# Kernel tuning notes

Hardware: AMD Instinct MI355X
Metric: run time of the kernel (lower is better)

## Reference

```python
import jax, jax.numpy as jnp
import numpy as np

N_HEAD, D_K, D_V, D_MODEL = 12, 64, 64, 768
SMOOTH = 1e-06
LN_EPS = 1e-06


def _layer_norm(x, g, b, eps=LN_EPS):
    m = x.mean(-1, keepdims=True)
    v = x.var(-1, keepdims=True)
    return (x - m) / jnp.sqrt(v + eps) * g + b


def setup_inputs() -> dict:
    key = jax.random.key(0)
    ks = jax.random.split(key, 12)
    b, L, R = 4, 1024, 97
    w = lambda k, i, o: jax.random.normal(k, (i, o), jnp.float32) * 0.02
    return {
        'doc_input': jax.random.normal(ks[0], (b, L, D_MODEL), jnp.float32),
        'rel_input': jax.random.normal(ks[1], (b, R, D_MODEL), jnp.float32),
        'mask': jax.random.randint(ks[2], (b, L), 0, 2, jnp.int32),
        'wq_doc': w(ks[3], D_MODEL, N_HEAD * D_K),
        'wk_doc': w(ks[4], D_MODEL, N_HEAD * D_K),
        'wv_doc': w(ks[5], D_MODEL, N_HEAD * D_V),
        'wk_rel': w(ks[6], D_MODEL, N_HEAD * D_K),
        'wv_rel': w(ks[7], D_MODEL, N_HEAD * D_V),
        'fc_doc': w(ks[8], N_HEAD * D_V, D_MODEL),
        'fc_rel': w(ks[9], N_HEAD * D_V, D_MODEL),
        'ln_doc_g': jnp.ones((D_MODEL,), jnp.float32),
        'ln_doc_b': jnp.zeros((D_MODEL,), jnp.float32),
        'ln_rel_g': jnp.ones((D_MODEL,), jnp.float32),
        'ln_rel_b': jnp.zeros((D_MODEL,), jnp.float32),
    }


def _forward(doc_input, rel_input, mask, wq_doc, wk_doc, wv_doc, wk_rel, wv_rel,
             fc_doc, fc_rel, ln_doc_g, ln_doc_b, ln_rel_g, ln_rel_b):
    b, L, _ = doc_input.shape
    R = rel_input.shape[1]
    proj = lambda x, w, d: (x @ w).reshape(x.shape[0], x.shape[1], N_HEAD, d).transpose(0, 2, 1, 3)
    dq = proj(doc_input, wq_doc, D_K)   # [b,h,L,dk]
    dk = proj(doc_input, wk_doc, D_K)
    dv = proj(doc_input, wv_doc, D_V)
    rk = proj(rel_input, wk_rel, D_K)   # [b,h,R,dk]
    rv = proj(rel_input, wv_rel, D_V)

    scale = 1.0 / np.sqrt(D_K).astype(np.float32)
    key_mask = (mask == 0)[:, None, None, :]  # [b,1,1,L]

    # doc-doc attention with relation-summed key fusion
    fused_k = dk + rk.sum(2, keepdims=True)  # broadcast [b,h,1,dk]
    scores = jnp.einsum('bhid,bhjd->bhij', dq, fused_k) * scale + SMOOTH
    scores = jnp.where(key_mask, -1e9, scores)
    alpha_dd = jax.nn.softmax(scores, axis=-1)  # dropout disabled (eval)

    # per-relation cross attention, batched over R (replaces python loop)
    rscores = jnp.einsum('bhrd,bhjd->bhrj', rk, dk) * scale + SMOOTH
    rscores = jnp.where(key_mask, -1e9, rscores)
    alpha_r = jax.nn.softmax(rscores, axis=-1)
    psi_r = jnp.einsum('bhrj,bhjd->bhrd', alpha_r, dv) + rv  # [b,h,R,dv]
    psi_r = psi_r.transpose(0, 2, 1, 3).reshape(b, R, N_HEAD * D_V)
    rel_output = _layer_norm(psi_r @ fc_rel + rel_input, ln_rel_g, ln_rel_b)

    fused_v = dv + rv.sum(2, keepdims=True)
    psi_i = jnp.einsum('bhij,bhjd->bhid', alpha_dd, fused_v)  # [b,h,L,dv]
    psi_i = psi_i.transpose(0, 2, 1, 3).reshape(b, L, N_HEAD * D_V)
    doc_output = _layer_norm(psi_i @ fc_doc + doc_input, ln_doc_g, ln_doc_b)
    return doc_output, rel_output


def reference(doc_input, rel_input, mask, wq_doc, wk_doc, wv_doc, wk_rel, wv_rel,
              fc_doc, fc_rel, ln_doc_g, ln_doc_b, ln_rel_g, ln_rel_b):
    return _forward(doc_input, rel_input, mask, wq_doc, wk_doc, wv_doc, wk_rel,
                    wv_rel, fc_doc, fc_rel, ln_doc_g, ln_doc_b, ln_rel_g, ln_rel_b)
```

## Files before the change

### kernel.cpp

```cpp
#include <hip/hip_runtime.h>
#include <hip/hip_bf16.h>

typedef __attribute__((ext_vector_type(8))) short bt8;
typedef __attribute__((ext_vector_type(4))) float f32x4;

__device__ __forceinline__ float bf2f(ushort u) {
    union { unsigned int i; float f; } v; v.i = ((unsigned int)u) << 16; return v.f;
}
__device__ __forceinline__ ushort f2bf(float f) {
    union { float f; unsigned int i; } v; v.f = f;
    unsigned int r = v.i + 0x7fffu + ((v.i >> 16) & 1u);
    return (ushort)(r >> 16);
}
__device__ __forceinline__ ushort f2bf_fast(float f) {
    __hip_bfloat16 h = __float2bfloat16(f);
    return reinterpret_cast<ushort&>(h);
}
__device__ __forceinline__ float fexp2(float x) { return __builtin_amdgcn_exp2f(x); }

#define GLOAD_LDS16(gp, lp) __builtin_amdgcn_global_load_lds( \
    (const __attribute__((address_space(1))) unsigned int*)(gp), \
    (__attribute__((address_space(3))) unsigned int*)(lp), 16, 0, 0)

__global__ __launch_bounds__(256) void cvt_two(
    const float* __restrict__ a, const float* __restrict__ b,
    ushort* __restrict__ oa, ushort* __restrict__ ob, int n1, int n2) {
    int i = blockIdx.x * 256 + threadIdx.x;
    if (i < n1) oa[i] = f2bf(a[i]);
    else if (i < n1 + n2) ob[i - n1] = f2bf(b[i - n1]);
}

__global__ void transpose_all(const float* __restrict__ p0, const float* __restrict__ p1,
                              const float* __restrict__ p2, const float* __restrict__ p3,
                              const float* __restrict__ p4, const float* __restrict__ p5,
                              const float* __restrict__ p6, ushort* __restrict__ out) {
    __shared__ float t[32][33];
    const float* W;
    switch (blockIdx.z) {
        case 0: W = p0; break; case 1: W = p1; break; case 2: W = p2; break;
        case 3: W = p3; break; case 4: W = p4; break; case 5: W = p5; break;
        default: W = p6; break;
    }
    ushort* WT = out + (size_t)blockIdx.z * 768 * 768;
    int bx = blockIdx.x * 32, by = blockIdx.y * 32;
    int x = threadIdx.x, y0 = threadIdx.y;
    for (int y = y0; y < 32; y += 8)
        t[y][x] = W[(size_t)(by + y) * 768 + bx + x];
    __syncthreads();
    for (int y = y0; y < 32; y += 8)
        WT[(size_t)(bx + y) * 768 + by + x] = f2bf(t[x][y]);
}

template<bool BF16O>
__global__ __launch_bounds__(256) void gemm_gl(
    const ushort* __restrict__ A, const ushort* __restrict__ BT,
    void* __restrict__ Cv, int M, int N, int K)
{
    __shared__ ushort As[128 * 32];
    __shared__ ushort Bs[128 * 32];
    const int tid = threadIdx.x;
    const int wave = tid >> 6, lane = tid & 63;
    const int row0 = blockIdx.x * 128, col0 = blockIdx.y * 128;
    const int wm = (wave >> 1) * 64, wn = (wave & 1) * 64;
    const int lr = lane & 15, lk = (lane >> 4) * 8;
    const int srow = wave * 16 + (lane >> 2);
    const int scol = (lane & 3) * 8;

    f32x4 acc[4][4];
    #pragma unroll
    for (int mi = 0; mi < 4; ++mi)
        #pragma unroll
        for (int ni = 0; ni < 4; ++ni)
            acc[mi][ni] = (f32x4){0.f, 0.f, 0.f, 0.f};

    int ar0 = row0 + srow;       if (ar0 >= M) ar0 = M - 1;
    int ar1 = row0 + 64 + srow;  if (ar1 >= M) ar1 = M - 1;
    const int bc0 = col0 + srow, bc1 = col0 + 64 + srow;

    for (int kt = 0; kt < K; kt += 32) {
        __syncthreads();
        GLOAD_LDS16(A + (size_t)ar0 * K + kt + scol, As + wave * 512);
        GLOAD_LDS16(A + (size_t)ar1 * K + kt + scol, As + 2048 + wave * 512);
        GLOAD_LDS16(BT + (size_t)bc0 * K + kt + scol, Bs + wave * 512);
        GLOAD_LDS16(BT + (size_t)bc1 * K + kt + scol, Bs + 2048 + wave * 512);
        __syncthreads();
        bt8 af[4], bf[4];
        #pragma unroll
        for (int mi = 0; mi < 4; ++mi)
            af[mi] = *(const bt8*)&As[(wm + mi * 16 + lr) * 32 + lk];
        #pragma unroll
        for (int ni = 0; ni < 4; ++ni)
            bf[ni] = *(const bt8*)&Bs[(wn + ni * 16 + lr) * 32 + lk];
        #pragma unroll
        for (int mi = 0; mi < 4; ++mi)
            #pragma unroll
            for (int ni = 0; ni < 4; ++ni)
                acc[mi][ni] = __builtin_amdgcn_mfma_f32_16x16x32_bf16(
                    af[mi], bf[ni], acc[mi][ni], 0, 0, 0);
    }

    #pragma unroll
    for (int mi = 0; mi < 4; ++mi) {
        int orow0 = row0 + wm + mi * 16 + (lane >> 4) * 4;
        #pragma unroll
        for (int ni = 0; ni < 4; ++ni) {
            int ocol = col0 + wn + ni * 16 + lr;
            if (ocol >= N) continue;
            #pragma unroll
            for (int r2 = 0; r2 < 4; ++r2) {
                int orow = orow0 + r2;
                if (orow < M) {
                    if (BF16O)
                        ((ushort*)Cv)[(size_t)orow * N + ocol] = f2bf(acc[mi][ni][r2]);
                    else
                        ((float*)Cv)[(size_t)orow * N + ocol] = acc[mi][ni][r2];
                }
            }
        }
    }
}

template<bool BF16O>
__global__ __launch_bounds__(256) void gemm64(
    const ushort* __restrict__ A, const ushort* __restrict__ BT,
    void* __restrict__ Cv, int M, int N, int K)
{
    __shared__ ushort As[64 * 32];
    __shared__ ushort Bs[64 * 32];
    const int tid = threadIdx.x;
    const int wave = tid >> 6, lane = tid & 63;
    const int row0 = blockIdx.x * 64, col0 = blockIdx.y * 64;
    const int wm = (wave >> 1) * 32, wn = (wave & 1) * 32;
    const int lr = lane & 15, lk = (lane >> 4) * 8;
    const int srow = tid >> 2;
    const int scol = (tid & 3) * 8;

    f32x4 acc[2][2];
    #pragma unroll
    for (int mi = 0; mi < 2; ++mi)
        #pragma unroll
        for (int ni = 0; ni < 2; ++ni)
            acc[mi][ni] = (f32x4){0.f, 0.f, 0.f, 0.f};

    int ar = row0 + srow; if (ar >= M) ar = M - 1;
    const int bc = col0 + srow;

    for (int kt = 0; kt < K; kt += 32) {
        __syncthreads();
        GLOAD_LDS16(A + (size_t)ar * K + kt + scol, As + wave * 512);
        GLOAD_LDS16(BT + (size_t)bc * K + kt + scol, Bs + wave * 512);
        __syncthreads();
        bt8 af[2], bf[2];
        #pragma unroll
        for (int mi = 0; mi < 2; ++mi)
            af[mi] = *(const bt8*)&As[(wm + mi * 16 + lr) * 32 + lk];
        #pragma unroll
        for (int ni = 0; ni < 2; ++ni)
            bf[ni] = *(const bt8*)&Bs[(wn + ni * 16 + lr) * 32 + lk];
        #pragma unroll
        for (int mi = 0; mi < 2; ++mi)
            #pragma unroll
            for (int ni = 0; ni < 2; ++ni)
                acc[mi][ni] = __builtin_amdgcn_mfma_f32_16x16x32_bf16(
                    af[mi], bf[ni], acc[mi][ni], 0, 0, 0);
    }

    #pragma unroll
    for (int mi = 0; mi < 2; ++mi) {
        int orow0 = row0 + wm + mi * 16 + (lane >> 4) * 4;
        #pragma unroll
        for (int ni = 0; ni < 2; ++ni) {
            int ocol = col0 + wn + ni * 16 + lr;
            if (ocol >= N) continue;
            #pragma unroll
            for (int r2 = 0; r2 < 4; ++r2) {
                int orow = orow0 + r2;
                if (orow < M) {
                    if (BF16O)
                        ((ushort*)Cv)[(size_t)orow * N + ocol] = f2bf(acc[mi][ni][r2]);
                    else
                        ((float*)Cv)[(size_t)orow * N + ocol] = acc[mi][ni][r2];
                }
            }
        }
    }
}

__global__ void relsum(const ushort* __restrict__ rkv,
                       float* __restrict__ rks, float* __restrict__ rvs) {
    int b = blockIdx.x;
    int c = blockIdx.y * 256 + threadIdx.x;
    float s1 = 0.f, s2 = 0.f;
    for (int r = 0; r < 97; ++r) {
        const ushort* row = rkv + (size_t)(b * 97 + r) * 1536;
        s1 += bf2f(row[c]);
        s2 += bf2f(row[768 + c]);
    }
    rks[b * 768 + c] = s1;
    rvs[b * 768 + c] = s2;
}

__global__ __launch_bounds__(256) void fusekv(
    const ushort* __restrict__ qkv, const float* __restrict__ rks,
    const float* __restrict__ rvs, ushort* __restrict__ kf, ushort* __restrict__ vf)
{
    int row = blockIdx.x;
    int c = blockIdx.y * 256 + threadIdx.x;
    int b = row >> 10;
    size_t qi = (size_t)row * 2304;
    size_t oi = (size_t)row * 768 + c;
    kf[oi] = f2bf(bf2f(qkv[qi + 768 + c]) + rks[b * 768 + c]);
    vf[oi] = f2bf(bf2f(qkv[qi + 1536 + c]) + rvs[b * 768 + c]);
}

#define SC2 0.18033688011112042f
#define THR2 10.0f

__global__ __launch_bounds__(256) void attn_mfma(
    const ushort* __restrict__ Qp, int qstride, size_t qbstride, int qmax,
    const ushort* __restrict__ Kp, const ushort* __restrict__ Vp,
    int kvstride, size_t kvbstride,
    const int* __restrict__ mask,
    float* __restrict__ Mo, float* __restrict__ Lo, ushort* __restrict__ Oo,
    int nspl, int ntiles, int qrows,
    ushort* __restrict__ psiD, int out_rows)
{
    __shared__ ushort Ks[64 * 64];
    __shared__ ushort Vt[64 * 64];
    __shared__ ushort Ps[4][16 * 64];
    __shared__ float  madd[64];
    ushort* Vlin = &Ps[0][0];

    const int tid = threadIdx.x;
    const int wv = tid >> 6, lane = tid & 63;
    const int lr = lane & 15, lk = (lane >> 4) * 8, rg = lane >> 4;
    const int bh = blockIdx.x, b = bh / 12, h = bh % 12;
    const int qb = blockIdx.y, spl = blockIdx.z;
    const int q0 = qb * 64 + wv * 16;

    const size_t kvbase = (size_t)b * kvbstride + h * 64;
    const size_t qbase  = (size_t)b * qbstride + h * 64;

    bt8 qf[2];
    {
        const int qi = q0 + lr;
        if (qi < qmax) {
            const ushort* qp = Qp + qbase + (size_t)qi * qstride + lk;
            qf[0] = *(const bt8*)qp;
            qf[1] = *(const bt8*)(qp + 32);
        } else {
            #pragma unroll
            for (int j = 0; j < 8; ++j) { qf[0][j] = 0; qf[1][j] = 0; }
        }
    }

    f32x4 acc[4];
    #pragma unroll
    for (int dg = 0; dg < 4; ++dg) acc[dg] = (f32x4){0.f, 0.f, 0.f, 0.f};
    float m_r[4], l_r[4];
    #pragma unroll
    for (int r = 0; r < 4; ++r) { m_r[r] = -3.0e38f; l_r[r] = 0.f; }

    const int key = tid >> 2, c0 = (tid & 3) * 16;
    const int vd = tid & 63, vw = tid >> 6;
    const int swk = (key & 7) << 3;
    const int swv = (vd & 7) << 3;
    const int swl = (lr & 7) << 3;

    for (int t = 0; t < ntiles; ++t) {
        const int k0 = (spl * ntiles + t) * 64;
        __syncthreads();
        {
            const ushort* src = Kp + kvbase + (size_t)(k0 + key) * kvstride + c0;
            int4 a = *(const int4*)src;
            int4 bq = *(const int4*)(src + 8);
            *(int4*)&Ks[key * 64 + (c0 ^ swk)] = a;
            *(int4*)&Ks[key * 64 + ((c0 + 8) ^ swk)] = bq;
        }
        {
            const ushort* src = Vp + kvbase + (size_t)(k0 + key) * kvstride + c0;
            int4 a = *(const int4*)src;
            int4 bq = *(const int4*)(src + 8);
            *(int4*)&Vlin[key * 64 + c0] = a;
            *(int4*)&Vlin[key * 64 + c0 + 8] = bq;
        }
        if (tid < 64)
            madd[tid] = (mask[b * 1024 + k0 + tid] == 0) ? -1e30f : 0.f;
        __syncthreads();

        {
            ushort tv[16];
            #pragma unroll
            for (int j = 0; j < 16; ++j) tv[j] = Vlin[(vw * 16 + j) * 64 + vd];
            const int cc = vw * 16;
            *(int4*)&Vt[vd * 64 + (cc ^ swv)] = *(int4*)tv;
            *(int4*)&Vt[vd * 64 + ((cc + 8) ^ swv)] = *(int4*)(tv + 8);
        }

        f32x4 sf[4];
        #pragma unroll
        for (int kg = 0; kg < 4; ++kg) {
            f32x4 s4 = (f32x4){0.f, 0.f, 0.f, 0.f};
            #pragma unroll
            for (int kk = 0; kk < 2; ++kk) {
                bt8 kf2 = *(const bt8*)&Ks[(kg * 16 + lr) * 64 + ((kk * 32 + lk) ^ swl)];
                s4 = __builtin_amdgcn_mfma_f32_16x16x32_bf16(qf[kk], kf2, s4, 0, 0, 0);
            }
            sf[kg] = s4;
        }

        const float ma0 = madd[lr], ma1 = madd[16 + lr];
        const float ma2 = madd[32 + lr], ma3 = madd[48 + lr];
        #pragma unroll
        for (int r = 0; r < 4; ++r) {
            float sv0 = sf[0][r] * SC2 + ma0;
            float sv1 = sf[1][r] * SC2 + ma1;
            float sv2 = sf[2][r] * SC2 + ma2;
            float sv3 = sf[3][r] * SC2 + ma3;
            float mx = fmaxf(fmaxf(sv0, sv1), fmaxf(sv2, sv3));
            mx = fmaxf(mx, __shfl_xor(mx, 1));
            mx = fmaxf(mx, __shfl_xor(mx, 2));
            mx = fmaxf(mx, __shfl_xor(mx, 4));
            mx = fmaxf(mx, __shfl_xor(mx, 8));
            float m_old = m_r[r];
            if (mx > m_old + THR2) {
                float corr = fexp2(m_old - mx);
                m_r[r] = mx;
                l_r[r] *= corr;
                #pragma unroll
                for (int dg = 0; dg < 4; ++dg) acc[dg][r] *= corr;
            }
            const float mn = m_r[r];
            float p0 = fexp2(sv0 - mn), p1 = fexp2(sv1 - mn);
            float p2 = fexp2(sv2 - mn), p3 = fexp2(sv3 - mn);
            float ps = (p0 + p1) + (p2 + p3);
            ps += __shfl_xor(ps, 1);
            ps += __shfl_xor(ps, 2);
            ps += __shfl_xor(ps, 4);
            ps += __shfl_xor(ps, 8);
            l_r[r] += ps;
            const int rowq = rg * 4 + r;
            const int swp = (rowq & 7) << 3;
            Ps[wv][rowq * 64 + ((0 * 16 + lr) ^ swp)] = f2bf_fast(p0);
            Ps[wv][rowq * 64 + ((1 * 16 + lr) ^ swp)] = f2bf_fast(p1);
            Ps[wv][rowq * 64 + ((2 * 16 + lr) ^ swp)] = f2bf_fast(p2);
            Ps[wv][rowq * 64 + ((3 * 16 + lr) ^ swp)] = f2bf_fast(p3);
        }

        __syncthreads();

        #pragma unroll
        for (int kk = 0; kk < 2; ++kk) {
            bt8 pa = *(const bt8*)&Ps[wv][lr * 64 + ((kk * 32 + lk) ^ swl)];
            #pragma unroll
            for (int dg = 0; dg < 4; ++dg) {
                bt8 vf2 = *(const bt8*)&Vt[(dg * 16 + lr) * 64 + ((kk * 32 + lk) ^ swl)];
                acc[dg] = __builtin_amdgcn_mfma_f32_16x16x32_bf16(pa, vf2, acc[dg], 0, 0, 0);
            }
        }
    }

    if (psiD) {
        #pragma unroll
        for (int r = 0; r < 4; ++r) {
            int qi = q0 + rg * 4 + r;
            if (qi >= qmax) continue;
            float rl = 1.f / l_r[r];
            size_t ob = ((size_t)b * out_rows + qi) * 768 + h * 64;
            #pragma unroll
            for (int dg = 0; dg < 4; ++dg)
                psiD[ob + dg * 16 + lr] = f2bf_fast(acc[dg][r] * rl);
        }
    } else {
        if (lr == 0) {
            #pragma unroll
            for (int r = 0; r < 4; ++r) {
                int qi = q0 + rg * 4 + r;
                int prow = (bh * nspl + spl) * qrows + qi;
                Mo[prow] = m_r[r];
                Lo[prow] = l_r[r];
            }
        }
        #pragma unroll
        for (int r = 0; r < 4; ++r) {
            int qi = q0 + rg * 4 + r;
            size_t orow = ((size_t)(bh * nspl + spl) * qrows + qi) * 64;
            #pragma unroll
            for (int dg = 0; dg < 4; ++dg)
                Oo[orow + dg * 16 + lr] = f2bf_fast(acc[dg][r]);
        }
    }
}

__global__ __launch_bounds__(64) void attn_merge(
    const float* __restrict__ Mo, const float* __restrict__ Lo, const ushort* __restrict__ Oo,
    const ushort* __restrict__ resid, size_t rbstride, int rstride,
    ushort* __restrict__ psi,
    int nspl, int qrows, int qmax, int out_rows)
{
    const int tid = threadIdx.x, bh = blockIdx.x, qb = blockIdx.y;
    const int b = bh / 12, h = bh % 12;
    const int qi = qb * 64 + tid;
    if (qi >= qmax) return;
    const int pb = bh * nspl;

    float M = -3.0e38f;
    for (int s = 0; s < nspl; ++s)
        M = fmaxf(M, Mo[(pb + s) * qrows + qi]);
    float L = 0.f, O[64];
    #pragma unroll
    for (int d = 0; d < 64; ++d) O[d] = 0.f;
    for (int s = 0; s < nspl; ++s) {
        int pr = (pb + s) * qrows + qi;
        float f = fexp2(Mo[pr] - M);
        L += Lo[pr] * f;
        const uint* op = (const uint*)(Oo + (size_t)pr * 64);
        #pragma unroll
        for (int d2 = 0; d2 < 32; ++d2) {
            uint u = op[d2];
            O[2*d2]   += f * bf2f((ushort)(u & 0xffffu));
            O[2*d2+1] += f * bf2f((ushort)(u >> 16));
        }
    }
    const float rl = 1.f / L;
    const size_t ob = ((size_t)b * out_rows + qi) * 768 + h * 64;
    if (resid) {
        const ushort* rp = resid + (size_t)b * rbstride + (size_t)qi * rstride + h * 64;
        #pragma unroll
        for (int d = 0; d < 64; ++d)
            psi[ob + d] = f2bf(O[d] * rl + bf2f(rp[d]));
    } else {
        #pragma unroll
        for (int d = 0; d < 64; ++d)
            psi[ob + d] = f2bf(O[d] * rl);
    }
}

__global__ __launch_bounds__(256) void ln_ker(
    const float* __restrict__ gin, const float* __restrict__ resid,
    const float* __restrict__ g, const float* __restrict__ bta,
    float* __restrict__ out)
{
    const int row = blockIdx.x, tid = threadIdx.x;
    const size_t rb = (size_t)row * 768;
    float x[3], s = 0.f, s2 = 0.f;
    #pragma unroll
    for (int k2 = 0; k2 < 3; ++k2) {
        int c = k2 * 256 + tid;
        float v = gin[rb + c] + resid[rb + c];
        x[k2] = v; s += v; s2 += v * v;
    }
    #pragma unroll
    for (int off = 32; off > 0; off >>= 1) {
        s  += __shfl_down(s, off);
        s2 += __shfl_down(s2, off);
    }
    __shared__ float red[10];
    const int wv = tid >> 6;
    if ((tid & 63) == 0) { red[wv] = s; red[4 + wv] = s2; }
    __syncthreads();
    if (tid == 0) {
        float ts = red[0] + red[1] + red[2] + red[3];
        float t2 = red[4] + red[5] + red[6] + red[7];
        float mean = ts * (1.f / 768.f);
        float var = t2 * (1.f / 768.f) - mean * mean;
        red[8] = mean;
        red[9] = rsqrtf(fmaxf(var, 0.f) + 1e-6f);
    }
    __syncthreads();
    const float mean = red[8], rstd = red[9];
    #pragma unroll
    for (int k2 = 0; k2 < 3; ++k2) {
        int c = k2 * 256 + tid;
        out[rb + c] = (x[k2] - mean) * rstd * g[c] + bta[c];
    }
}

extern "C" void kernel_launch(void* const* d_in, const int* in_sizes, int n_in,
                              void* d_out, int out_size, void* d_ws, size_t ws_size,
                              hipStream_t stream) {
    const float* doc  = (const float*)d_in[0];
    const float* rel  = (const float*)d_in[1];
    const int*   mask = (const int*)d_in[2];
    const float* ln_dg = (const float*)d_in[10];
    const float* ln_db = (const float*)d_in[11];
    const float* ln_rg = (const float*)d_in[12];
    const float* ln_rb = (const float*)d_in[13];

    char* ws = (char*)d_ws;
    size_t off = 0;
    ushort* wtall = (ushort*)(ws + off); off += (size_t)7 * 768 * 768 * 2;
    ushort* wtqkv = wtall;
    ushort* wt34  = wtall + (size_t)3 * 768 * 768;
    ushort* wt5   = wtall + (size_t)5 * 768 * 768;
    ushort* wt6   = wtall + (size_t)6 * 768 * 768;
    ushort* doc_bf = (ushort*)(ws + off); off += (size_t)4096 * 768 * 2;
    ushort* rel_bf = (ushort*)(ws + off); off += (size_t)388 * 768 * 2;
    ushort* qkv_bf = (ushort*)(ws + off); off += (size_t)4096 * 2304 * 2;
    ushort* rkv_bf = (ushort*)(ws + off); off += (size_t)388 * 1536 * 2;
    float*  rks = (float*)(ws + off); off += (size_t)4 * 768 * 4;
    float*  rvs = (float*)(ws + off); off += (size_t)4 * 768 * 4;
    ushort* kf_bf = (ushort*)(ws + off); off += (size_t)4096 * 768 * 2;
    ushort* vf_bf = (ushort*)(ws + off); off += (size_t)4096 * 768 * 2;
    ushort* psi_i = (ushort*)(ws + off); off += (size_t)4096 * 768 * 2;
    ushort* psi_r = (ushort*)(ws + off); off += (size_t)388 * 768 * 2;
    float*  Mo = (float*)(ws + off);  off += (size_t)48 * 8 * 128 * 4;
    float*  Lo = (float*)(ws + off);  off += (size_t)48 * 8 * 128 * 4;
    ushort* Oo = (ushort*)(ws + off); off += (size_t)48 * 8 * 128 * 64 * 2;
    float*  gdoc = (float*)(ws + off); off += (size_t)4096 * 768 * 4;
    float*  grel = (float*)(ws + off); off += (size_t)388 * 768 * 4;

    float* out_doc = (float*)d_out;
    float* out_rel = out_doc + (size_t)4096 * 768;

    const int n1 = 4096 * 768, n2 = 388 * 768;
    cvt_two<<<dim3((n1 + n2 + 255) / 256), 256, 0, stream>>>(doc, rel, doc_bf, rel_bf, n1, n2);
    transpose_all<<<dim3(24, 24, 7), dim3(32, 8), 0, stream>>>(
        (const float*)d_in[3], (const float*)d_in[4], (const float*)d_in[5],
        (const float*)d_in[6], (const float*)d_in[7], (const float*)d_in[8],
        (const float*)d_in[9], wtall);

    gemm_gl<true><<<dim3(32, 18), 256, 0, stream>>>(doc_bf, wtqkv, qkv_bf, 4096, 2304, 768);
    gemm64<true><<<dim3(7, 24),  256, 0, stream>>>(rel_bf, wt34, rkv_bf, 388, 1536, 768);

    relsum<<<dim3(4, 3), 256, 0, stream>>>(rkv_bf, rks, rvs);
    fusekv<<<dim3(4096, 3), 256, 0, stream>>>(qkv_bf, rks, rvs, kf_bf, vf_bf);

    attn_mfma<<<dim3(48, 2, 8), 256, 0, stream>>>(
        rkv_bf, 1536, (size_t)97 * 1536, 97,
        qkv_bf + 768, qkv_bf + 1536, 2304, (size_t)1024 * 2304,
        mask, Mo, Lo, Oo, 8, 2, 128, (ushort*)nullptr, 0);
    attn_merge<<<dim3(48, 2), 64, 0, stream>>>(
        Mo, Lo, Oo, rkv_bf + 768, (size_t)97 * 1536, 1536, psi_r, 8, 128, 97, 97);

    attn_mfma<<<dim3(48, 16, 1), 256, 0, stream>>>(
        qkv_bf, 2304, (size_t)1024 * 2304, 1024,
        kf_bf, vf_bf, 768, (size_t)1024 * 768,
        mask, Mo, Lo, Oo, 1, 16, 1024, psi_i, 1024);

    gemm64<false><<<dim3(64, 12), 256, 0, stream>>>(psi_i, wt5, gdoc, 4096, 768, 768);
    gemm64<false><<<dim3(7, 12),  256, 0, stream>>>(psi_r, wt6, grel, 388, 768, 768);

    ln_ker<<<4096, 256, 0, stream>>>(gdoc, doc, ln_dg, ln_db, out_doc);
    ln_ker<<<388,  256, 0, stream>>>(grel, rel, ln_rg, ln_rb, out_rel);
}
```

Baseline: 188.4 us.

## Prefetch next K/V tile into registers and load V transposed directly

Result: slower. 206.8 us (+9.8%).

```diff
diff --git a/kernel.cpp b/kernel.cpp
--- a/kernel.cpp
+++ b/kernel.cpp
@@ -229,7 +229,6 @@
     __shared__ ushort Vt[64 * 64];
     __shared__ ushort Ps[4][16 * 64];
     __shared__ float  madd[64];
-    ushort* Vlin = &Ps[0][0];
 
     const int tid = threadIdx.x;
     const int wv = tid >> 6, lane = tid & 63;
@@ -267,35 +266,41 @@
     const int swv = (vd & 7) << 3;
     const int swl = (lr & 7) << 3;
 
+    int4 kA, kB;
+    union { ushort u16[16]; int4 v4[2]; } vu;
+
+    {
+        const int k0 = spl * ntiles * 64;
+        const ushort* src = Kp + kvbase + (size_t)(k0 + key) * kvstride + c0;
+        kA = *(const int4*)src;
+        kB = *(const int4*)(src + 8);
+        const ushort* vsrc = Vp + kvbase + (size_t)(k0 + vw * 16) * kvstride + vd;
+        #pragma unroll
+        for (int j = 0; j < 16; ++j) vu.u16[j] = vsrc[(size_t)j * kvstride];
+    }
+
     for (int t = 0; t < ntiles; ++t) {
         const int k0 = (spl * ntiles + t) * 64;
         __syncthreads();
+        *(int4*)&Ks[key * 64 + (c0 ^ swk)] = kA;
+        *(int4*)&Ks[key * 64 + ((c0 + 8) ^ swk)] = kB;
         {
-            const ushort* src = Kp + kvbase + (size_t)(k0 + key) * kvstride + c0;
-            int4 a = *(const int4*)src;
-            int4 bq = *(const int4*)(src + 8);
-            *(int4*)&Ks[key * 64 + (c0 ^ swk)] = a;
-            *(int4*)&Ks[key * 64 + ((c0 + 8) ^ swk)] = bq;
-        }
-        {
-            const ushort* src = Vp + kvbase + (size_t)(k0 + key) * kvstride + c0;
-            int4 a = *(const int4*)src;
-            int4 bq = *(const int4*)(src + 8);
-            *(int4*)&Vlin[key * 64 + c0] = a;
-            *(int4*)&Vlin[key * 64 + c0 + 8] = bq;
+            const int cc = vw * 16;
+            *(int4*)&Vt[vd * 64 + (cc ^ swv)] = vu.v4[0];
+            *(int4*)&Vt[vd * 64 + ((cc + 8) ^ swv)] = vu.v4[1];
         }
         if (tid < 64)
             madd[tid] = (mask[b * 1024 + k0 + tid] == 0) ? -1e30f : 0.f;
+        if (t + 1 < ntiles) {
+            const int k1 = k0 + 64;
+            const ushort* src = Kp + kvbase + (size_t)(k1 + key) * kvstride + c0;
+            kA = *(const int4*)src;
+            kB = *(const int4*)(src + 8);
+            const ushort* vsrc = Vp + kvbase + (size_t)(k1 + vw * 16) * kvstride + vd;
+            #pragma unroll
+            for (int j = 0; j < 16; ++j) vu.u16[j] = vsrc[(size_t)j * kvstride];
+        }
         __syncthreads();
-
-        {
-            ushort tv[16];
-            #pragma unroll
-            for (int j = 0; j < 16; ++j) tv[j] = Vlin[(vw * 16 + j) * 64 + vd];
-            const int cc = vw * 16;
-            *(int4*)&Vt[vd * 64 + (cc ^ swv)] = *(int4*)tv;
-            *(int4*)&Vt[vd * 64 + ((cc + 8) ^ swv)] = *(int4*)(tv + 8);
-        }
 
         f32x4 sf[4];
         #pragma unroll
@@ -347,8 +352,6 @@
             Ps[wv][rowq * 64 + ((3 * 16 + lr) ^ swp)] = f2bf_fast(p3);
         }
 
-        __syncthreads();
-
         #pragma unroll
         for (int kk = 0; kk < 2; ++kk) {
             bt8 pa = *(const bt8*)&Ps[wv][lr * 64 + ((kk * 32 + lk) ^ swl)];
```
